# Optimization experiments

Measured on AMD Instinct MI355X. Metric: run time of the kernel, lower is better.

## Reference

```python
import jax, jax.numpy as jnp
import numpy as np

M, IN, OUT = 8192, 4096, 4096
XOR_MASK = (1 << 3) | (1 << 7)  # 0x88: flips sign bit of each packed nibble


def _dequant_int4(weight_packed, weight_scales):
    """Decode packed int4 weights (offset-binary nibbles) to scaled float.

    weight_packed: [OUT, IN//2] int32, each byte holds two nibbles (v+8).
    Low nibble -> even input column, high nibble -> odd input column.
    """
    w = jnp.bitwise_xor(weight_packed, XOR_MASK)  # offset-binary -> two's complement nibbles
    low = jnp.bitwise_and(w, 0xF)
    high = jnp.bitwise_and(jnp.right_shift(w, 4), 0xF)
    low = jnp.where(low >= 8, low - 16, low)    # signed int4 in [-8, 7]
    high = jnp.where(high >= 8, high - 16, high)
    # interleave nibbles: [OUT, IN//2, 2] -> [OUT, IN]
    deq = jnp.stack([low, high], axis=-1).reshape(weight_packed.shape[0], -1)
    return deq.astype(weight_scales.dtype) * weight_scales[:, None]  # [OUT, IN]


def setup_inputs() -> dict:
    key = jax.random.key(0)
    k1, k2, k3, k4 = jax.random.split(key, 4)
    x = jax.random.normal(k1, (M, IN), dtype=jnp.float32)
    weight_packed = jax.random.randint(k2, (OUT, IN // 2), 0, 256, dtype=jnp.int32)
    weight_scales = jax.random.uniform(k3, (OUT,), dtype=jnp.float32) * 0.02 + 1e-3
    bias = jax.random.normal(k4, (OUT,), dtype=jnp.float32)
    return {"x": x, "weight_packed": weight_packed,
            "weight_scales": weight_scales, "bias": bias}


def reference(x, weight_packed, weight_scales, bias):
    # w4a16 forward: dequantize int4 weights per output row, then GEMM + bias.
    w = _dequant_int4(weight_packed, weight_scales)  # [OUT, IN]
    return jnp.dot(x, w.T) + bias  # [M, OUT]
```

## Files before the change

kernel.cpp:

```cpp
#include <hip/hip_runtime.h>
#include <cstdint>
#include <cstddef>

#define M_DIM 8192
#define K_DIM 4096
#define N_DIM 4096

typedef unsigned short u16;
typedef __bf16 bf16x8 __attribute__((ext_vector_type(8)));
typedef u16 u16x8 __attribute__((ext_vector_type(8)));
typedef float f32x4 __attribute__((ext_vector_type(4)));

__device__ __forceinline__ u16 f2bf_rne(float f) {
  uint32_t u = __builtin_bit_cast(uint32_t, f);
  return (u16)((u + 0x7FFFu + ((u >> 16) & 1u)) >> 16);
}
__device__ __forceinline__ u16 i2bf(int i) {
  return (u16)(__builtin_bit_cast(uint32_t, (float)i) >> 16);
}

#define XBLKS 16384
#define WBLKS 8192

__global__ __launch_bounds__(256) void prep(const float* __restrict__ x,
                                            const int* __restrict__ wp,
                                            u16* __restrict__ xb,
                                            u16* __restrict__ wb) {
  const int b = blockIdx.x;
  if (b < XBLKS) {
    size_t t = (size_t)b * 256 + threadIdx.x;
    const float4* xp = (const float4*)x;
    float4 a = xp[2 * t];
    float4 c = xp[2 * t + 1];
    u16x8 r;
    r[0] = f2bf_rne(a.x); r[1] = f2bf_rne(a.y); r[2] = f2bf_rne(a.z); r[3] = f2bf_rne(a.w);
    r[4] = f2bf_rne(c.x); r[5] = f2bf_rne(c.y); r[6] = f2bf_rne(c.z); r[7] = f2bf_rne(c.w);
    ((u16x8*)xb)[t] = r;
  } else {
    size_t t = (size_t)(b - XBLKS) * 256 + threadIdx.x;
    int4 p = ((const int4*)wp)[t];
    u16x8 r;
    int v;
    v = p.x ^ 0x88; r[0] = i2bf((v << 28) >> 28); r[1] = i2bf((v << 24) >> 28);
    v = p.y ^ 0x88; r[2] = i2bf((v << 28) >> 28); r[3] = i2bf((v << 24) >> 28);
    v = p.z ^ 0x88; r[4] = i2bf((v << 28) >> 28); r[5] = i2bf((v << 24) >> 28);
    v = p.w ^ 0x88; r[6] = i2bf((v << 28) >> 28); r[7] = i2bf((v << 24) >> 28);
    ((u16x8*)wb)[t] = r;
  }
}

__global__ __launch_bounds__(256, 2) void gemm_bt_w4a16(
    const u16* __restrict__ A,
    const u16* __restrict__ B,
    const float* __restrict__ scales,
    const float* __restrict__ bias,
    float* __restrict__ C) {
  __shared__ u16 sA[128 * 64];
  __shared__ u16 sB[128 * 64];

  const int tid = threadIdx.x;
  const int lane = tid & 63;
  const int wave = tid >> 6;
  const int m0 = blockIdx.y * 128;
  const int n0 = blockIdx.x * 128;
  const int wm = (wave & 1) * 64;
  const int wn = (wave >> 1) * 64;
  const int lrow = lane & 15;
  const int quad = lane >> 4;

  f32x4 acc[4][4] = {};

  const int srow = tid >> 3;
  const int key = srow & 7;
  const int schunk = ((tid & 7) ^ key) * 8;
  const u16* ga = A + (size_t)(m0 + srow) * K_DIM + schunk;
  const u16* gb = B + (size_t)(n0 + srow) * K_DIM + schunk;

  for (int kb = 0; kb < K_DIM; kb += 64) {
    __syncthreads();
#pragma unroll
    for (int r = 0; r < 4; ++r) {
      __builtin_amdgcn_global_load_lds(
          (const __attribute__((address_space(1))) void*)(ga + (size_t)(r * 32) * K_DIM + kb),
          (__attribute__((address_space(3))) void*)((char*)sA + wave * 1024 + r * 4096),
          16, 0, 0);
    }
#pragma unroll
    for (int r = 0; r < 4; ++r) {
      __builtin_amdgcn_global_load_lds(
          (const __attribute__((address_space(1))) void*)(gb + (size_t)(r * 32) * K_DIM + kb),
          (__attribute__((address_space(3))) void*)((char*)sB + wave * 1024 + r * 4096),
          16, 0, 0);
    }
    __syncthreads();

#pragma unroll
    for (int s = 0; s < 2; ++s) {
      u16x8 af[4], bfr[4];
#pragma unroll
      for (int i = 0; i < 4; ++i)
        af[i] = *(const u16x8*)(sA + (wm + i * 16 + lrow) * 64 +
                                ((s * 4 + quad) ^ (lrow & 7)) * 8);
#pragma unroll
      for (int j = 0; j < 4; ++j)
        bfr[j] = *(const u16x8*)(sB + (wn + j * 16 + lrow) * 64 +
                                 ((s * 4 + quad) ^ (lrow & 7)) * 8);
#pragma unroll
      for (int i = 0; i < 4; ++i)
#pragma unroll
        for (int j = 0; j < 4; ++j)
          acc[i][j] = __builtin_amdgcn_mfma_f32_16x16x32_bf16(
              __builtin_bit_cast(bf16x8, af[i]),
              __builtin_bit_cast(bf16x8, bfr[j]), acc[i][j], 0, 0, 0);
    }
  }

#pragma unroll
  for (int j = 0; j < 4; ++j) {
    const int n = n0 + wn + j * 16 + lrow;
    const float sc = scales[n];
    const float bi = bias[n];
#pragma unroll
    for (int i = 0; i < 4; ++i) {
#pragma unroll
      for (int r = 0; r < 4; ++r) {
        const int m = m0 + wm + i * 16 + quad * 4 + r;
        C[(size_t)m * N_DIM + n] = acc[i][j][r] * sc + bi;
      }
    }
  }
}

__global__ __launch_bounds__(256) void fallback_w4a16(
    const float* __restrict__ x, const int* __restrict__ wp,
    const float* __restrict__ scales, const float* __restrict__ bias,
    float* __restrict__ out) {
  const int n = blockIdx.x * 256 + threadIdx.x;
  const int m = blockIdx.y;
  const float* xr = x + (size_t)m * K_DIM;
  const int* wr = wp + (size_t)n * (K_DIM / 2);
  float acc = 0.f;
  for (int j = 0; j < K_DIM / 2; ++j) {
    int w = wr[j] ^ 0x88;
    float lo = (float)((w << 28) >> 28);
    float hi = (float)((w << 24) >> 28);
    acc += xr[2 * j] * lo + xr[2 * j + 1] * hi;
  }
  out[(size_t)m * N_DIM + n] = acc * scales[n] + bias[n];
}

extern "C" void kernel_launch(void* const* d_in, const int* in_sizes, int n_in,
                              void* d_out, int out_size, void* d_ws, size_t ws_size,
                              hipStream_t stream) {
  const float* x = (const float*)d_in[0];
  const int* wp = (const int*)d_in[1];
  const float* sc = (const float*)d_in[2];
  const float* bi = (const float*)d_in[3];
  float* out = (float*)d_out;

  const size_t xb_elems = (size_t)M_DIM * K_DIM;
  const size_t wb_elems = (size_t)N_DIM * K_DIM;
  const size_t need = (xb_elems + wb_elems) * sizeof(u16);

  if (ws_size >= need) {
    u16* xb = (u16*)d_ws;
    u16* wb = xb + xb_elems;
    prep<<<XBLKS + WBLKS, 256, 0, stream>>>(x, wp, xb, wb);
    gemm_bt_w4a16<<<dim3(N_DIM / 128, M_DIM / 128), 256, 0, stream>>>(xb, wb, sc, bi, out);
  } else {
    fallback_w4a16<<<dim3(N_DIM / 256, M_DIM), 256, 0, stream>>>(x, wp, sc, bi, out);
  }
}
```

Measured before the change: 478.5 us.

## Double-buffer LDS tiles with K-step 32 and prefetch the next tile

Splits the shared-memory A and B tiles into two 32-wide K buffers. The loads for the next K slice are issued into the other buffer while MFMAs run on the current one, and each iteration now needs only one barrier instead of two. The load mapping and XOR swizzle are adapted to 64-byte rows. The intent is to hide global-to-LDS latency behind compute. In exchange there are twice as many loop iterations, each doing half the MFMA work. The compiler may also insert conservative waits on the async loads before the LDS reads, which would serialize them again.

```diff
diff --git a/kernel.cpp b/kernel.cpp
--- a/kernel.cpp
+++ b/kernel.cpp
@@ -55,8 +55,8 @@
     const float* __restrict__ scales,
     const float* __restrict__ bias,
     float* __restrict__ C) {
-  __shared__ u16 sA[128 * 64];
-  __shared__ u16 sB[128 * 64];
+  __shared__ u16 sA[2][128 * 32];
+  __shared__ u16 sB[2][128 * 32];
 
   const int tid = threadIdx.x;
   const int lane = tid & 63;
@@ -67,53 +67,60 @@
   const int wn = (wave >> 1) * 64;
   const int lrow = lane & 15;
   const int quad = lane >> 4;
+  const int rkey = (lrow >> 1) & 3;
 
   f32x4 acc[4][4] = {};
 
-  const int srow = tid >> 3;
-  const int key = srow & 7;
-  const int schunk = ((tid & 7) ^ key) * 8;
+  const int srow = tid >> 2;
+  const int skey = (tid >> 3) & 3;
+  const int schunk = ((tid & 3) ^ skey) * 8;
   const u16* ga = A + (size_t)(m0 + srow) * K_DIM + schunk;
   const u16* gb = B + (size_t)(n0 + srow) * K_DIM + schunk;
 
-  for (int kb = 0; kb < K_DIM; kb += 64) {
+#define ISSUE_TILE(kb_, p_)                                                      \
+  do {                                                                           \
+    _Pragma("unroll")                                                            \
+    for (int r = 0; r < 2; ++r) {                                                \
+      __builtin_amdgcn_global_load_lds(                                          \
+          (const __attribute__((address_space(1))) void*)(ga + (size_t)(r * 64) * K_DIM + (kb_)), \
+          (__attribute__((address_space(3))) void*)((char*)&sA[(p_)][0] + tid * 16 + r * 4096),   \
+          16, 0, 0);                                                             \
+    }                                                                            \
+    _Pragma("unroll")                                                            \
+    for (int r = 0; r < 2; ++r) {                                                \
+      __builtin_amdgcn_global_load_lds(                                          \
+          (const __attribute__((address_space(1))) void*)(gb + (size_t)(r * 64) * K_DIM + (kb_)), \
+          (__attribute__((address_space(3))) void*)((char*)&sB[(p_)][0] + tid * 16 + r * 4096),   \
+          16, 0, 0);                                                             \
+    }                                                                            \
+  } while (0)
+
+  ISSUE_TILE(0, 0);
+  int p = 0;
+#pragma unroll 2
+  for (int kb = 0; kb < K_DIM; kb += 32) {
     __syncthreads();
+    if (kb + 32 < K_DIM) ISSUE_TILE(kb + 32, p ^ 1);
+
+    const u16* bufA = &sA[p][0];
+    const u16* bufB = &sB[p][0];
+    u16x8 af[4], bfr[4];
 #pragma unroll
-    for (int r = 0; r < 4; ++r) {
-      __builtin_amdgcn_global_load_lds(
-          (const __attribute__((address_space(1))) void*)(ga + (size_t)(r * 32) * K_DIM + kb),
-          (__attribute__((address_space(3))) void*)((char*)sA + wave * 1024 + r * 4096),
-          16, 0, 0);
-    }
+    for (int i = 0; i < 4; ++i)
+      af[i] = *(const u16x8*)(bufA + (wm + i * 16 + lrow) * 32 + (quad ^ rkey) * 8);
 #pragma unroll
-    for (int r = 0; r < 4; ++r) {
-      __builtin_amdgcn_global_load_lds(
-          (const __attribute__((address_space(1))) void*)(gb + (size_t)(r * 32) * K_DIM + kb),
-          (__attribute__((address_space(3))) void*)((char*)sB + wave * 1024 + r * 4096),
-          16, 0, 0);
-    }
-    __syncthreads();
-
+    for (int j = 0; j < 4; ++j)
+      bfr[j] = *(const u16x8*)(bufB + (wn + j * 16 + lrow) * 32 + (quad ^ rkey) * 8);
 #pragma unroll
-    for (int s = 0; s < 2; ++s) {
-      u16x8 af[4], bfr[4];
-#pragma unroll
-      for (int i = 0; i < 4; ++i)
-        af[i] = *(const u16x8*)(sA + (wm + i * 16 + lrow) * 64 +
-                                ((s * 4 + quad) ^ (lrow & 7)) * 8);
+    for (int i = 0; i < 4; ++i)
 #pragma unroll
       for (int j = 0; j < 4; ++j)
-        bfr[j] = *(const u16x8*)(sB + (wn + j * 16 + lrow) * 64 +
-                                 ((s * 4 + quad) ^ (lrow & 7)) * 8);
-#pragma unroll
-      for (int i = 0; i < 4; ++i)
-#pragma unroll
-        for (int j = 0; j < 4; ++j)
-          acc[i][j] = __builtin_amdgcn_mfma_f32_16x16x32_bf16(
-              __builtin_bit_cast(bf16x8, af[i]),
-              __builtin_bit_cast(bf16x8, bfr[j]), acc[i][j], 0, 0, 0);
-    }
+        acc[i][j] = __builtin_amdgcn_mfma_f32_16x16x32_bf16(
+            __builtin_bit_cast(bf16x8, af[i]),
+            __builtin_bit_cast(bf16x8, bfr[j]), acc[i][j], 0, 0, 0);
+    p ^= 1;
   }
+#undef ISSUE_TILE
 
 #pragma unroll
   for (int j = 0; j < 4; ++j) {
```

New measurement: 536.2 us. 1.12x slower.
